# Kernel tuning notes

Hardware: AMD Instinct MI355X
Metric: run time of the kernel (lower is better)

The kernel has to match this reference:

```python
import jax, jax.numpy as jnp
import numpy as np

N, H, W, DIM = 16, 64, 64, 256
HEADS, ANCH = 8, 8
HD = DIM // HEADS  # 32


def setup_inputs() -> dict:
    key = jax.random.key(0)
    ks = jax.random.split(key, 5)
    s = 0.02
    return {
        "x": jax.random.normal(ks[0], (N, H, W, DIM), jnp.float32),
        "W_proj": jax.random.normal(ks[1], (2 * DIM, DIM), jnp.float32) * s,
        "b_proj": jax.random.normal(ks[2], (2 * DIM,), jnp.float32) * s,
        "W_out": jax.random.normal(ks[3], (DIM, DIM), jnp.float32) * s,
        "b_out": jax.random.normal(ks[4], (DIM,), jnp.float32) * s,
        "alpha": jnp.ones((1,), jnp.float32),
        "beta": jnp.zeros((1,), jnp.float32),
    }


def _l2norm(v, axis):
    # matches torch F.normalize(dim=axis, eps=1e-12)
    return v / jnp.maximum(jnp.linalg.norm(v, axis=axis, keepdims=True), 1e-12)


def reference(x, W_proj, b_proj, W_out, b_out, alpha, beta):
    n, h, w, dim = x.shape
    heads, a = HEADS, ANCH
    hd = dim // heads
    m = n * heads
    # proj -> (n,h,w,2*dim) -> (n,2*dim,h,w) -> (m, 2*hd, h, w)
    xp = (x @ W_proj.T + b_proj).transpose(0, 3, 1, 2).reshape(m, 2 * hd, h, w)
    flat = xp.reshape(m, 2 * hd, h * w)
    point0, value0 = flat[:, :hd], flat[:, hd:]          # (m, hd, hw) each
    # adaptive max pool to (a,a); h,w divisible by a so uniform windows
    pooled = xp.reshape(m, 2 * hd, a, h // a, a, w // a).max(axis=(3, 5))
    pooled = pooled.reshape(m, 2 * hd, a * a)
    point1, value1 = pooled[:, :hd], pooled[:, hd:]      # (m, hd, a2) each
    point0, point1 = _l2norm(point0, 1), _l2norm(point1, 1)
    # cosine similarity: (m, hw, a2)
    sim = jnp.einsum('mdp,mda->mpa', point0, point1)
    sim = jax.nn.sigmoid(alpha[0] * sim + beta[0])
    # hard top-1 routing over anchors
    idx = jnp.argmax(sim, axis=-1)                       # (m, hw)
    sim = jax.nn.one_hot(idx, a * a, dtype=sim.dtype) * sim  # (m, hw, a2)
    # aggregate values into anchors: sum_p value0[m,d,p]*sim[m,p,a] + value1
    agg = jnp.einsum('mdp,mpa->mda', value0, sim) + value1   # (m, hd, a2)
    agg = agg / (sim.sum(axis=1)[:, None, :] + 1.0)
    # broadcast back to points: sum_a sim[m,p,a]*agg[m,d,a]
    msg = jnp.einsum('mpa,mda->mdp', sim, agg)               # (m, hd, hw)
    msg = msg.reshape(n, dim, h, w).transpose(0, 2, 3, 1)    # (n,h,w,dim)
    return msg @ W_out.T + b_out
```

## Files before the change

kernel.cpp:

```cpp
#include <hip/hip_runtime.h>
#include <float.h>
#include <math.h>


#define NPIX   4096
#define NIMG   16
#define TOTPIX 65536
#define DIM2   512

typedef __attribute__((ext_vector_type(8))) short bf16x8;
typedef __attribute__((ext_vector_type(4))) float f32x4;

#define BM 128
#define BN 128
#define BK 32

__global__ __launch_bounds__(512, 2) void proj_point(
    const float* __restrict__ X, const float* __restrict__ W,
    const float* __restrict__ bias, float* __restrict__ XP) {
  __shared__ float As[BK][BM];
  __shared__ float Bs[BK][BN];
  const int tid = threadIdx.x;
  const int M0 = blockIdx.x * BM, C0 = blockIdx.y * BN;
  const int tm = tid >> 5, tn = tid & 31;

  const int r = tid & 127;
  const int kq = (tid >> 7) << 3;

  const int pcr = C0 + r;
  const float* Xa = X + (size_t)(M0 + r) * 256 + kq;
  const float* Wb = W + (size_t)((pcr >> 5) * 64 + (pcr & 31)) * 256 + kq;

  float4 xa0, xa1, wb0, wb1;

#define LOADT(ko)                                                      \
  do {                                                                 \
    xa0 = *(const float4*)(Xa + (ko));                                 \
    xa1 = *(const float4*)(Xa + (ko) + 4);                             \
    wb0 = *(const float4*)(Wb + (ko));                                 \
    wb1 = *(const float4*)(Wb + (ko) + 4);                             \
  } while (0)

  float acc[8][4];
#pragma unroll
  for (int i = 0; i < 8; ++i)
#pragma unroll
    for (int j = 0; j < 4; ++j) acc[i][j] = 0.f;

  LOADT(0);

  for (int k0 = 0; k0 < 256; k0 += BK) {
    __syncthreads();
#pragma unroll
    for (int j = 0; j < 4; ++j) {
      As[kq + j][r]     = (&xa0.x)[j];
      As[kq + 4 + j][r] = (&xa1.x)[j];
      Bs[kq + j][r]     = (&wb0.x)[j];
      Bs[kq + 4 + j][r] = (&wb1.x)[j];
    }
    __syncthreads();
    if (k0 + BK < 256) LOADT(k0 + BK);
#pragma unroll
    for (int kk = 0; kk < BK; ++kk) {
      float a[8], b[4];
      *(float4*)&a[0] = *(const float4*)&As[kk][tm * 8];
      *(float4*)&a[4] = *(const float4*)&As[kk][tm * 8 + 4];
      *(float4*)&b[0] = *(const float4*)&Bs[kk][tn * 4];
#pragma unroll
      for (int i = 0; i < 8; ++i)
#pragma unroll
        for (int j = 0; j < 4; ++j)
          acc[i][j] = fmaf(a[i], b[j], acc[i][j]);
    }
  }

  const int c = C0 + tn * 4;
  const int pcol = (c >> 5) * 64 + (c & 31);
  const float4 bq = *(const float4*)(bias + pcol);
#pragma unroll
  for (int i = 0; i < 8; ++i) {
    const size_t row = (size_t)(M0 + tm * 8 + i) * DIM2 + pcol;
    float4 o;
    o.x = acc[i][0] + bq.x; o.y = acc[i][1] + bq.y;
    o.z = acc[i][2] + bq.z; o.w = acc[i][3] + bq.w;
    *(float4*)(XP + row) = o;
  }
}

__device__ __forceinline__ void split2(float x, unsigned short& h1,
                                       unsigned short& h2) {
  unsigned u1 = __float_as_uint(x);
  h1 = (unsigned short)(u1 >> 16);
  float r1 = x - __uint_as_float(u1 & 0xFFFF0000u);
  h2 = (unsigned short)(__float_as_uint(r1) >> 16);
}

__global__ __launch_bounds__(256, 2) void proj_value(
    const float* __restrict__ X, const float* __restrict__ W,
    const float* __restrict__ bias, float* __restrict__ XP) {
  __shared__ unsigned char lds[4 * 8192];
  const int tid = threadIdx.x;
  const int M0 = blockIdx.x * 128;
  const int V0 = blockIdx.y * 128;

  const int w = tid >> 6, l = tid & 63;
  const int wm = w >> 1, wn = w & 1;

  const int jj = tid & 7;
  const int rsub = tid >> 3;

  const float* Xbase = X + (size_t)M0 * 256;

  float4 ra[4], rb[4];
#define GLOADV(kofs)                                                          \
  do {                                                                        \
    _Pragma("unroll") for (int i = 0; i < 4; ++i) {                           \
      ra[i] = *(const float4*)(Xbase + (size_t)(i * 32 + rsub) * 256 + (kofs) + jj * 4); \
      rb[i] = *(const float4*)(W + (size_t)((((V0 >> 5) + i) * 64) + 32 + rsub) * 256 + (kofs) + jj * 4); \
    }                                                                         \
  } while (0)

  f32x4 acc[4][4] = {};

  const int fr = l & 15, kg = l >> 4;
  const int chunk = kg << 4;

  GLOADV(0);

  for (int s = 0; s < 8; ++s) {
    __syncthreads();
#pragma unroll
    for (int i = 0; i < 4; ++i) {
      const int row = i * 32 + rsub;
      const int off = row * 64 + jj * 8;
      unsigned short a1[4], a2[4], b1[4], b2[4];
#pragma unroll
      for (int e = 0; e < 4; ++e) {
        split2(((const float*)&ra[i])[e], a1[e], a2[e]);
        split2(((const float*)&rb[i])[e], b1[e], b2[e]);
      }
#define PK2(arr) make_uint2((unsigned)(arr)[0] | ((unsigned)(arr)[1] << 16),  \
                            (unsigned)(arr)[2] | ((unsigned)(arr)[3] << 16))
      *(uint2*)(lds + 0 * 8192 + off) = PK2(a1);
      *(uint2*)(lds + 1 * 8192 + off) = PK2(a2);
      *(uint2*)(lds + 2 * 8192 + off) = PK2(b1);
      *(uint2*)(lds + 3 * 8192 + off) = PK2(b2);
#undef PK2
    }
    __syncthreads();
    if (s < 7) GLOADV((s + 1) * 32);

    bf16x8 af[4][2];
#pragma unroll
    for (int mi = 0; mi < 4; ++mi) {
      const int base = (wm * 64 + mi * 16 + fr) * 64 + chunk;
      af[mi][0] = *(const bf16x8*)(lds + 0 * 8192 + base);
      af[mi][1] = *(const bf16x8*)(lds + 1 * 8192 + base);
    }
#pragma unroll
    for (int ni = 0; ni < 4; ++ni) {
      const int base = (wn * 64 + ni * 16 + fr) * 64 + chunk;
      const bf16x8 b1 = *(const bf16x8*)(lds + 2 * 8192 + base);
      const bf16x8 b2 = *(const bf16x8*)(lds + 3 * 8192 + base);
#pragma unroll
      for (int mi = 0; mi < 4; ++mi) {
        f32x4 c = acc[mi][ni];
        c = __builtin_amdgcn_mfma_f32_16x16x32_bf16(af[mi][0], b1, c, 0, 0, 0);
        c = __builtin_amdgcn_mfma_f32_16x16x32_bf16(af[mi][0], b2, c, 0, 0, 0);
        c = __builtin_amdgcn_mfma_f32_16x16x32_bf16(af[mi][1], b1, c, 0, 0, 0);
        acc[mi][ni] = c;
      }
    }
  }

  const int orow0 = M0 + wm * 64 + (l >> 4) * 4;
#pragma unroll
  for (int ni = 0; ni < 4; ++ni) {
    const int vc = V0 + wn * 64 + ni * 16 + fr;
    const int pcol = (vc >> 5) * 64 + 32 + (vc & 31);
    const float bv = bias[pcol];
#pragma unroll
    for (int mi = 0; mi < 4; ++mi)
#pragma unroll
      for (int j = 0; j < 4; ++j)
        XP[(size_t)(orow0 + mi * 16 + j) * DIM2 + pcol] = acc[mi][ni][j] + bv;
  }
}

__device__ __forceinline__ void pool_emit(float v, int C, int n, int a,
                                          float* __restrict__ P1N,
                                          float* __restrict__ V1) {
  const int h = C >> 6, cc = C & 63;
  const int m = n * 8 + h;
  const bool isPoint = cc < 32;
  float sq = isPoint ? v * v : 0.f;
#pragma unroll
  for (int o = 16; o > 0; o >>= 1) sq += __shfl_xor(sq, o, 32);
  if (isPoint) {
    const float rn = 1.0f / fmaxf(sqrtf(sq), 1e-12f);
    P1N[((size_t)m * 64 + a) * 32 + cc] = v * rn;
  } else {
    V1[((size_t)m * 64 + a) * 32 + (cc - 32)] = v;
  }
}

__global__ __launch_bounds__(256) void pool_norm(
    const float* __restrict__ XP, float* __restrict__ P1N,
    float* __restrict__ V1) {
  const int n = blockIdx.x, a = blockIdx.y;
  const int ay = a >> 3, ax = a & 7;
  const int tid = threadIdx.x;
  const size_t base = ((size_t)n * NPIX + (size_t)(ay * 8) * 64 + ax * 8) * DIM2;
  float m0 = -FLT_MAX, m1 = -FLT_MAX;
#pragma unroll
  for (int iy = 0; iy < 8; ++iy) {
    const float* rowp = XP + base + (size_t)iy * 64 * DIM2;
#pragma unroll
    for (int ix = 0; ix < 8; ++ix) {
      m0 = fmaxf(m0, rowp[(size_t)ix * DIM2 + tid]);
      m1 = fmaxf(m1, rowp[(size_t)ix * DIM2 + tid + 256]);
    }
  }
  pool_emit(m0, tid, n, a, P1N, V1);
  pool_emit(m1, tid + 256, n, a, P1N, V1);
}

__global__ __launch_bounds__(256) void sim_argmax(
    const float* __restrict__ XP, const float* __restrict__ P1N,
    const float* __restrict__ alpha, const float* __restrict__ beta,
    float* __restrict__ SV, int* __restrict__ IDX) {
  const int m = blockIdx.x, chunk = blockIdx.y;
  const int n = m >> 3, h = m & 7;
  __shared__ float P1[64][32];
  const int tid = threadIdx.x;
  {
    const float4* src = (const float4*)(P1N + (size_t)m * 2048);
    float4* dst = (float4*)&P1[0][0];
    dst[tid] = src[tid];
    dst[tid + 256] = src[tid + 256];
  }
  __syncthreads();
  const float al = alpha[0], be = beta[0];

  const int p0 = chunk * 256 + tid;
  const int p1 = p0 + 2048;
  const float* row0 = XP + ((size_t)n * NPIX + p0) * DIM2 + h * 64;
  const float* row1 = XP + ((size_t)n * NPIX + p1) * DIM2 + h * 64;

  float v0[32], v1[32];
#pragma unroll
  for (int q = 0; q < 8; ++q) {
    float4 t0 = ((const float4*)row0)[q];
    float4 t1 = ((const float4*)row1)[q];
    v0[q * 4 + 0] = t0.x; v0[q * 4 + 1] = t0.y; v0[q * 4 + 2] = t0.z; v0[q * 4 + 3] = t0.w;
    v1[q * 4 + 0] = t1.x; v1[q * 4 + 1] = t1.y; v1[q * 4 + 2] = t1.z; v1[q * 4 + 3] = t1.w;
  }
  float ss0 = 0.f, ss1 = 0.f;
#pragma unroll
  for (int d = 0; d < 32; ++d) { ss0 += v0[d] * v0[d]; ss1 += v1[d] * v1[d]; }
  const float rn0 = 1.0f / fmaxf(sqrtf(ss0), 1e-12f);
  const float rn1 = 1.0f / fmaxf(sqrtf(ss1), 1e-12f);
#pragma unroll
  for (int d = 0; d < 32; ++d) { v0[d] *= rn0; v1[d] *= rn1; }

  float best0 = -1.f, best1 = -1.f;
  int bi0 = 0, bi1 = 0;
  for (int a = 0; a < 64; ++a) {
    float d0a = 0.f, d0b = 0.f, d1a = 0.f, d1b = 0.f;
#pragma unroll
    for (int d = 0; d < 16; ++d) {
      const float wa = P1[a][2 * d], wb = P1[a][2 * d + 1];
      d0a = fmaf(v0[2 * d], wa, d0a);
      d0b = fmaf(v0[2 * d + 1], wb, d0b);
      d1a = fmaf(v1[2 * d], wa, d1a);
      d1b = fmaf(v1[2 * d + 1], wb, d1b);
    }
    const float t0 = al * (d0a + d0b) + be;
    const float t1 = al * (d1a + d1b) + be;
    const float s0 = 1.0f / (1.0f + expf(-t0));
    const float s1 = 1.0f / (1.0f + expf(-t1));
    if (s0 > best0) { best0 = s0; bi0 = a; }
    if (s1 > best1) { best1 = s1; bi1 = a; }
  }
  SV[(size_t)m * NPIX + p0] = best0;
  IDX[(size_t)m * NPIX + p0] = bi0;
  SV[(size_t)m * NPIX + p1] = best1;
  IDX[(size_t)m * NPIX + p1] = bi1;
}

#define NSEG 4
__global__ __launch_bounds__(256) void scatter_partial(
    const float* __restrict__ XP, const float* __restrict__ SV,
    const int* __restrict__ IDX, float* __restrict__ PART) {
  const int m = blockIdx.x, seg = blockIdx.y;
  const int n = m >> 3, h = m & 7;
  __shared__ float agg[8][32][65];
  __shared__ float ssum[8][64];
  const int tid = threadIdx.x;
  const int g = tid >> 5, d = tid & 31;

  for (int e = tid; e < 8 * 32 * 65; e += 256) ((float*)agg)[e] = 0.f;
  for (int e = tid; e < 8 * 64; e += 256) ((float*)ssum)[e] = 0.f;
  __syncthreads();

  const size_t svbase = (size_t)m * NPIX;
  const int pbase = seg * 1024 + g * 128;
  int lastid = -1;
  float acc = 0.f, accS = 0.f;
  for (int i = 0; i < 128; ++i) {
    const int p = pbase + i;
    const float sv = SV[svbase + p];
    const int id = IDX[svbase + p];
    const float vv = XP[((size_t)n * NPIX + p) * DIM2 + h * 64 + 32 + d];
    if (id != lastid) {
      if (lastid >= 0) {
        agg[g][d][lastid] += acc;
        if (d == 0) ssum[g][lastid] += accS;
      }
      lastid = id; acc = 0.f; accS = 0.f;
    }
    acc = fmaf(vv, sv, acc);
    accS += sv;
  }
  if (lastid >= 0) {
    agg[g][d][lastid] += acc;
    if (d == 0) ssum[g][lastid] += accS;
  }
  __syncthreads();

  float* P = PART + (size_t)(m * NSEG + seg) * 2112;
  for (int e = tid; e < 2048; e += 256) {
    const int dd = e >> 6, aa = e & 63;
    float s = 0.f;
#pragma unroll
    for (int gg = 0; gg < 8; ++gg) s += agg[gg][dd][aa];
    P[e] = s;
  }
  if (tid < 64) {
    float s = 0.f;
#pragma unroll
    for (int gg = 0; gg < 8; ++gg) s += ssum[gg][tid];
    P[2048 + tid] = s;
  }
}

__global__ __launch_bounds__(256) void reduce_proj(
    const float* __restrict__ PART, const float* __restrict__ V1,
    const float* __restrict__ Wout, float* __restrict__ PA) {
  const int m = blockIdx.x;
  const int h = m & 7;
  __shared__ float aggF[64][33];
  __shared__ float ssumF[64];
  const int tid = threadIdx.x;
  const float* P = PART + (size_t)m * NSEG * 2112;

  if (tid < 64) {
    float s = 0.f;
#pragma unroll
    for (int seg = 0; seg < NSEG; ++seg) s += P[seg * 2112 + 2048 + tid];
    ssumF[tid] = s + 1.0f;
  }
  __syncthreads();

  for (int e = tid; e < 2048; e += 256) {
    const int dd = e >> 6, aa = e & 63;
    float s = 0.f;
#pragma unroll
    for (int seg = 0; seg < NSEG; ++seg) s += P[seg * 2112 + e];
    s += V1[((size_t)m * 64 + aa) * 32 + dd];
    aggF[aa][dd] = s / ssumF[aa];
  }
  __syncthreads();

  float w[32];
  const float* wrow = Wout + (size_t)tid * 256 + h * 32;
#pragma unroll
  for (int q = 0; q < 8; ++q) {
    const float4 t = ((const float4*)wrow)[q];
    w[q * 4 + 0] = t.x; w[q * 4 + 1] = t.y; w[q * 4 + 2] = t.z; w[q * 4 + 3] = t.w;
  }
  for (int aa = 0; aa < 64; ++aa) {
    float s0 = 0.f, s1 = 0.f;
#pragma unroll
    for (int d2 = 0; d2 < 16; ++d2) {
      s0 = fmaf(w[2 * d2], aggF[aa][2 * d2], s0);
      s1 = fmaf(w[2 * d2 + 1], aggF[aa][2 * d2 + 1], s1);
    }
    PA[((size_t)m * 64 + aa) * 256 + tid] = s0 + s1;
  }
}

__global__ __launch_bounds__(256) void out_assemble(
    const float* __restrict__ PA, const float* __restrict__ SV,
    const int* __restrict__ IDX, const float* __restrict__ bout,
    float* __restrict__ OUT) {
  const int tid = threadIdx.x;
  const int lp = tid >> 6, lane = tid & 63;
  const size_t p = (size_t)blockIdx.x * 4 + lp;
  const int n = (int)(p >> 12);
  const int pp = (int)(p & 4095);
  float4 acc = ((const float4*)bout)[lane];
#pragma unroll
  for (int h = 0; h < 8; ++h) {
    const int m = n * 8 + h;
    const float sv = SV[(size_t)m * NPIX + pp];
    const int id = IDX[(size_t)m * NPIX + pp];
    const float4 pa = ((const float4*)(PA + ((size_t)m * 64 + id) * 256))[lane];
    acc.x = fmaf(sv, pa.x, acc.x);
    acc.y = fmaf(sv, pa.y, acc.y);
    acc.z = fmaf(sv, pa.z, acc.z);
    acc.w = fmaf(sv, pa.w, acc.w);
  }
  ((float4*)OUT)[p * 64 + lane] = acc;
}

extern "C" void kernel_launch(void* const* d_in, const int* in_sizes, int n_in,
                              void* d_out, int out_size, void* d_ws, size_t ws_size,
                              hipStream_t stream) {
  const float* x     = (const float*)d_in[0];
  const float* Wp    = (const float*)d_in[1];
  const float* bp    = (const float*)d_in[2];
  const float* Wo    = (const float*)d_in[3];
  const float* bo    = (const float*)d_in[4];
  const float* alpha = (const float*)d_in[5];
  const float* beta  = (const float*)d_in[6];
  float* out = (float*)d_out;

  char* ws = (char*)d_ws;
  float* XP   = (float*)(ws);
  float* P1N  = (float*)(ws + 134217728u);
  float* V1   = (float*)(ws + 135266304u);
  float* SVv  = (float*)(ws + 136314880u);
  int*   IDX  = (int*)  (ws + 138412032u);
  float* PA   = (float*)(ws + 140509184u);
  float* PART = (float*)(ws + 148897792u);
  (void)in_sizes; (void)n_in; (void)out_size; (void)ws_size;

  proj_point     <<<dim3(512, 2), 512, 0, stream>>>(x, Wp, bp, XP);
  proj_value     <<<dim3(512, 2), 256, 0, stream>>>(x, Wp, bp, XP);
  pool_norm      <<<dim3(16, 64), 256, 0, stream>>>(XP, P1N, V1);
  sim_argmax     <<<dim3(128, 8), 256, 0, stream>>>(XP, P1N, alpha, beta, SVv, IDX);
  scatter_partial<<<dim3(128, NSEG), 256, 0, stream>>>(XP, SVv, IDX, PART);
  reduce_proj    <<<128, 256, 0, stream>>>(PART, V1, Wo, PA);
  out_assemble   <<<16384, 256, 0, stream>>>(PA, SVv, IDX, bo, out);
}
```

Before: 342.7 us.

## Double-buffer projection GEMM LDS and vectorize pool and scatter loads

The FP32 projection GEMM now uses two LDS buffers, so the next tile is written while the current one is consumed, with one barrier per k-step instead of two. The pool kernel loads two channels per thread as float2 and does a 16-lane shuffle reduction with float2 stores. The scatter kernel reads SV and IDX as float4/int4 and batches four value loads before the run-length accumulation. This targets barrier stalls and scalar memory instructions, at the cost of doubled LDS in proj_point, which may reduce occupancy.

```diff
diff --git a/kernel.cpp b/kernel.cpp
--- a/kernel.cpp
+++ b/kernel.cpp
@@ -18,8 +18,8 @@
 __global__ __launch_bounds__(512, 2) void proj_point(
     const float* __restrict__ X, const float* __restrict__ W,
     const float* __restrict__ bias, float* __restrict__ XP) {
-  __shared__ float As[BK][BM];
-  __shared__ float Bs[BK][BN];
+  __shared__ float As[2][BK][BM];
+  __shared__ float Bs[2][BK][BN];
   const int tid = threadIdx.x;
   const int M0 = blockIdx.x * BM, C0 = blockIdx.y * BN;
   const int tm = tid >> 5, tn = tid & 31;
@@ -41,6 +41,16 @@
     wb1 = *(const float4*)(Wb + (ko) + 4);                             \
   } while (0)
 
+#define WRITEB(bf)                                                     \
+  do {                                                                 \
+    _Pragma("unroll") for (int j = 0; j < 4; ++j) {                    \
+      As[bf][kq + j][r]     = (&xa0.x)[j];                             \
+      As[bf][kq + 4 + j][r] = (&xa1.x)[j];                             \
+      Bs[bf][kq + j][r]     = (&wb0.x)[j];                             \
+      Bs[bf][kq + 4 + j][r] = (&wb1.x)[j];                             \
+    }                                                                  \
+  } while (0)
+
   float acc[8][4];
 #pragma unroll
   for (int i = 0; i < 8; ++i)
@@ -48,30 +58,29 @@
     for (int j = 0; j < 4; ++j) acc[i][j] = 0.f;
 
   LOADT(0);
-
-  for (int k0 = 0; k0 < 256; k0 += BK) {
-    __syncthreads();
-#pragma unroll
-    for (int j = 0; j < 4; ++j) {
-      As[kq + j][r]     = (&xa0.x)[j];
-      As[kq + 4 + j][r] = (&xa1.x)[j];
-      Bs[kq + j][r]     = (&wb0.x)[j];
-      Bs[kq + 4 + j][r] = (&wb1.x)[j];
-    }
-    __syncthreads();
-    if (k0 + BK < 256) LOADT(k0 + BK);
+  WRITEB(0);
+  LOADT(BK);
+  __syncthreads();
+
+  for (int t = 0; t < 8; ++t) {
+    const int cur = t & 1;
+    if (t < 7) {
+      WRITEB(cur ^ 1);
+      if (t < 6) LOADT((t + 2) * BK);
+    }
 #pragma unroll
     for (int kk = 0; kk < BK; ++kk) {
       float a[8], b[4];
-      *(float4*)&a[0] = *(const float4*)&As[kk][tm * 8];
-      *(float4*)&a[4] = *(const float4*)&As[kk][tm * 8 + 4];
-      *(float4*)&b[0] = *(const float4*)&Bs[kk][tn * 4];
+      *(float4*)&a[0] = *(const float4*)&As[cur][kk][tm * 8];
+      *(float4*)&a[4] = *(const float4*)&As[cur][kk][tm * 8 + 4];
+      *(float4*)&b[0] = *(const float4*)&Bs[cur][kk][tn * 4];
 #pragma unroll
       for (int i = 0; i < 8; ++i)
 #pragma unroll
         for (int j = 0; j < 4; ++j)
           acc[i][j] = fmaf(a[i], b[j], acc[i][j]);
     }
+    __syncthreads();
   }
 
   const int c = C0 + tn * 4;
@@ -187,23 +196,6 @@
   }
 }
 
-__device__ __forceinline__ void pool_emit(float v, int C, int n, int a,
-                                          float* __restrict__ P1N,
-                                          float* __restrict__ V1) {
-  const int h = C >> 6, cc = C & 63;
-  const int m = n * 8 + h;
-  const bool isPoint = cc < 32;
-  float sq = isPoint ? v * v : 0.f;
-#pragma unroll
-  for (int o = 16; o > 0; o >>= 1) sq += __shfl_xor(sq, o, 32);
-  if (isPoint) {
-    const float rn = 1.0f / fmaxf(sqrtf(sq), 1e-12f);
-    P1N[((size_t)m * 64 + a) * 32 + cc] = v * rn;
-  } else {
-    V1[((size_t)m * 64 + a) * 32 + (cc - 32)] = v;
-  }
-}
-
 __global__ __launch_bounds__(256) void pool_norm(
     const float* __restrict__ XP, float* __restrict__ P1N,
     float* __restrict__ V1) {
@@ -211,18 +203,35 @@
   const int ay = a >> 3, ax = a & 7;
   const int tid = threadIdx.x;
   const size_t base = ((size_t)n * NPIX + (size_t)(ay * 8) * 64 + ax * 8) * DIM2;
+  const int c0 = tid * 2;
   float m0 = -FLT_MAX, m1 = -FLT_MAX;
 #pragma unroll
   for (int iy = 0; iy < 8; ++iy) {
     const float* rowp = XP + base + (size_t)iy * 64 * DIM2;
 #pragma unroll
     for (int ix = 0; ix < 8; ++ix) {
-      m0 = fmaxf(m0, rowp[(size_t)ix * DIM2 + tid]);
-      m1 = fmaxf(m1, rowp[(size_t)ix * DIM2 + tid + 256]);
-    }
-  }
-  pool_emit(m0, tid, n, a, P1N, V1);
-  pool_emit(m1, tid + 256, n, a, P1N, V1);
+      const float2 v = *(const float2*)(rowp + (size_t)ix * DIM2 + c0);
+      m0 = fmaxf(m0, v.x);
+      m1 = fmaxf(m1, v.y);
+    }
+  }
+  const int m = n * 8 + (tid >> 5);
+  const int l32 = tid & 31;
+  float s0 = m0 * m0, s1 = m1 * m1;
+#pragma unroll
+  for (int o = 8; o > 0; o >>= 1) {
+    s0 += __shfl_xor(s0, o, 32);
+    s1 += __shfl_xor(s1, o, 32);
+  }
+  const float sq = s0 + s1;
+  if (l32 < 16) {
+    const float rn = 1.0f / fmaxf(sqrtf(sq), 1e-12f);
+    float2 o2; o2.x = m0 * rn; o2.y = m1 * rn;
+    *(float2*)(P1N + ((size_t)m * 64 + a) * 32 + 2 * l32) = o2;
+  } else {
+    float2 o2; o2.x = m0; o2.y = m1;
+    *(float2*)(V1 + ((size_t)m * 64 + a) * 32 + 2 * (l32 - 16)) = o2;
+  }
 }
 
 __global__ __launch_bounds__(256) void sim_argmax(
@@ -307,20 +316,28 @@
   const int pbase = seg * 1024 + g * 128;
   int lastid = -1;
   float acc = 0.f, accS = 0.f;
-  for (int i = 0; i < 128; ++i) {
-    const int p = pbase + i;
-    const float sv = SV[svbase + p];
-    const int id = IDX[svbase + p];
-    const float vv = XP[((size_t)n * NPIX + p) * DIM2 + h * 64 + 32 + d];
-    if (id != lastid) {
-      if (lastid >= 0) {
-        agg[g][d][lastid] += acc;
-        if (d == 0) ssum[g][lastid] += accS;
+  for (int i0 = 0; i0 < 128; i0 += 4) {
+    const int p = pbase + i0;
+    const float4 sv4 = *(const float4*)(SV + svbase + p);
+    const int4 id4 = *(const int4*)(IDX + svbase + p);
+    float vv4[4];
+#pragma unroll
+    for (int j = 0; j < 4; ++j)
+      vv4[j] = XP[((size_t)n * NPIX + p + j) * DIM2 + h * 64 + 32 + d];
+#pragma unroll
+    for (int j = 0; j < 4; ++j) {
+      const float sv = (&sv4.x)[j];
+      const int id = (&id4.x)[j];
+      if (id != lastid) {
+        if (lastid >= 0) {
+          agg[g][d][lastid] += acc;
+          if (d == 0) ssum[g][lastid] += accS;
+        }
+        lastid = id; acc = 0.f; accS = 0.f;
       }
-      lastid = id; acc = 0.f; accS = 0.f;
-    }
-    acc = fmaf(vv, sv, acc);
-    accS += sv;
+      acc = fmaf(vv4[j], sv, acc);
+      accS += sv;
+    }
   }
   if (lastid >= 0) {
     agg[g][d][lastid] += acc;
```

After: 342.8 us. No clear change (+0.0%).
